# Kernel optimization log

Measured on AMD Instinct MI355X. Metric: run time of the kernel, lower is better.

## Reference

```python
import jax, jax.numpy as jnp
import numpy as np
from jax import lax

# pywt db8 decomposition low-pass filter (dec_lo), 16 taps
DB8_DEC_LO = jnp.array([
    -0.00011747678400228192, 0.0006754494059985568, -0.0003917403729959771,
    -0.00487035299301066, 0.008746094047015655, 0.013981027917015516,
    -0.04408825393106472, -0.01736930100202211, 0.128747426620186,
    0.00047248457399797254, -0.2840155429624281, -0.015829105256023893,
    0.5853546836548691, 0.6756307362980128, 0.3128715909144659,
    0.05441584224308161], dtype=jnp.float32)

FLEN = 16


def dwt2_ll(x):
    """LL band of pywt.dwt2(x, 'db8', mode='symmetric') for x [B,C,H,W].
    pywt dwt along an axis == symmetric pad by flen-1, full correlation with
    reversed dec_lo, take every other sample starting at offset 1."""
    B, C, H, W = x.shape
    f = DB8_DEC_LO[::-1]  # np.convolve flips the filter -> correlate with reversed
    xr = x.reshape(B * C, 1, H, W)
    # along W
    p = jnp.pad(xr, ((0, 0), (0, 0), (0, 0), (FLEN - 1, FLEN - 1)), mode='symmetric')[..., 1:]
    y = lax.conv_general_dilated(p, f.reshape(1, 1, 1, FLEN), (1, 2), 'VALID',
                                 dimension_numbers=('NCHW', 'OIHW', 'NCHW'))
    # along H
    p = jnp.pad(y, ((0, 0), (0, 0), (FLEN - 1, FLEN - 1), (0, 0)), mode='symmetric')[:, :, 1:, :]
    z = lax.conv_general_dilated(p, f.reshape(1, 1, FLEN, 1), (2, 1), 'VALID',
                                 dimension_numbers=('NCHW', 'OIHW', 'NCHW'))
    return z.reshape(B, C, z.shape[2], z.shape[3])


def setup_inputs() -> dict:
    key = jax.random.key(0)
    k1, k2, k3, k4 = jax.random.split(key, 4)
    B, C, H, W = 8, 128, 256, 256
    r = 16
    x = jax.random.normal(k1, (B, C, H, W), jnp.float32)
    conv_w = jax.random.normal(k2, (1, 2, 7, 7), jnp.float32) * 0.1  # SpatialAttention conv, no bias
    fc_w1 = jax.random.normal(k3, (C // r, C), jnp.float32) * (1.0 / np.sqrt(C))
    fc_w2 = jax.random.normal(k4, (C, C // r), jnp.float32) * (1.0 / np.sqrt(C // r))
    weight = jnp.array(0.0, dtype=jnp.float32)  # learnable fusion scalar
    return {"x": x, "conv_w": conv_w, "fc_w1": fc_w1, "fc_w2": fc_w2, "weight": weight}


def reference(x, conv_w, fc_w1, fc_w2, weight):
    # --- spatial attention ---
    avg = jnp.mean(x, axis=1, keepdims=True)
    mx = jnp.max(x, axis=1, keepdims=True)
    s = jnp.concatenate([avg, mx], axis=1)  # [B,2,H,W]
    attn = jax.nn.sigmoid(lax.conv_general_dilated(
        s, conv_w, (1, 1), ((3, 3), (3, 3)),
        dimension_numbers=('NCHW', 'OIHW', 'NCHW')))  # [B,1,H,W]
    spatial_out = x * attn
    # --- wavelet (frequency) attention; LL detached in the original ---
    ll = lax.stop_gradient(dwt2_ll(x))  # [B,C,H',W']
    y = jnp.mean(ll, axis=(2, 3))  # global avg pool -> [B,C]
    h = jax.nn.relu(y @ fc_w1.T)
    w = jax.nn.sigmoid(h @ fc_w2.T)[:, :, None, None]  # [B,C,1,1]
    wavelet_out = x * w
    # --- gated fusion ---
    alpha = jax.nn.sigmoid(weight)
    out = alpha * spatial_out + (1.0 - alpha) * wavelet_out
    return out, attn, w, alpha
```

## Files before the change

kernel.cpp:

```cpp
#include <hip/hip_runtime.h>
#include <math.h>

#define BB 8
#define CC 128
#define HH 256
#define WW 256
#define HWD 65536
#define NOUT (67108864)

#define ATTN_OFF ((size_t)NOUT)
#define W_OFF (ATTN_OFF + (size_t)BB * HWD)
#define ALPHA_OFF (W_OFF + (size_t)BB * CC)

__constant__ float g_declo[16] = {
    -0.00011747678400228192f, 0.0006754494059985568f, -0.0003917403729959771f,
    -0.00487035299301066f,    0.008746094047015655f,  0.013981027917015516f,
    -0.04408825393106472f,    -0.01736930100202211f,  0.128747426620186f,
    0.00047248457399797254f,  -0.2840155429624281f,   -0.015829105256023893f,
    0.5853546836548691f,      0.6756307362980128f,    0.3128715909144659f,
    0.05441584224308161f};

__device__ __forceinline__ float sigmoidf_(float v) {
    return 1.0f / (1.0f + expf(-v));
}

__device__ __forceinline__ float a_weight(int t) {
    float v = 0.0f;
    for (int k = (t & 1); k < 16; k += 2) v += g_declo[15 - k];
    if (t <= 13) {
        for (int k = 13 - t; k >= 0; k -= 2) v += g_declo[15 - k];
    }
    if (t >= 242) {
        for (int k = 257 - t; k < 16; k += 2) v += g_declo[15 - k];
    }
    return v;
}

__global__ __launch_bounds__(256) void pass1_kernel(
    const float* __restrict__ x, float* __restrict__ avg_s,
    float* __restrict__ max_s, float* __restrict__ partial) {
    const int blk = blockIdx.x;
    const int b = blk >> 8;
    const int h = blk & 255;
    const int tid = threadIdx.x;
    const int wv = tid >> 6;
    const int lane = tid & 63;

    __shared__ __align__(16) float a_sh[256];
    __shared__ float dotc[CC];
    __shared__ __align__(16) float lsum[4][256];
    __shared__ __align__(16) float lmax[4][256];
    __shared__ float T[4][64][17];

    a_sh[tid] = a_weight(tid);
    __syncthreads();

    const float4 a4 = reinterpret_cast<const float4*>(a_sh)[lane];
    const float ah = a_sh[h];

    float4 sum4 = {0.f, 0.f, 0.f, 0.f};
    float4 max4 = {-INFINITY, -INFINITY, -INFINITY, -INFINITY};

    const size_t base = (size_t)b * CC * HWD + (size_t)h * WW + (lane << 2);

    for (int g = 0; g < 2; ++g) {
        const int cbase = (wv << 5) + (g << 4);
        float dots[16];
#pragma unroll
        for (int i = 0; i < 16; ++i) {
            const float4 v = *reinterpret_cast<const float4*>(
                x + base + (size_t)(cbase + i) * HWD);
            dots[i] = a4.x * v.x + a4.y * v.y + a4.z * v.z + a4.w * v.w;
            sum4.x += v.x; sum4.y += v.y; sum4.z += v.z; sum4.w += v.w;
            max4.x = fmaxf(max4.x, v.x); max4.y = fmaxf(max4.y, v.y);
            max4.z = fmaxf(max4.z, v.z); max4.w = fmaxf(max4.w, v.w);
        }
#pragma unroll
        for (int i = 0; i < 16; ++i) T[wv][lane][i] = dots[i];
        const int cr = lane & 15;
        const int q = lane >> 4;
        float s = 0.f;
#pragma unroll
        for (int j = 0; j < 16; ++j) s += T[wv][(q << 4) + j][cr];
        s += __shfl_xor(s, 16, 64);
        s += __shfl_xor(s, 32, 64);
        if (lane < 16) dotc[cbase + lane] = s;
    }

    reinterpret_cast<float4*>(&lsum[wv][0])[lane] = sum4;
    reinterpret_cast<float4*>(&lmax[wv][0])[lane] = max4;
    __syncthreads();

    const int col = tid;
    const float s = lsum[0][col] + lsum[1][col] + lsum[2][col] + lsum[3][col];
    const float m = fmaxf(fmaxf(lmax[0][col], lmax[1][col]),
                          fmaxf(lmax[2][col], lmax[3][col]));
    const size_t po = (size_t)b * HWD + (size_t)h * WW + col;
    avg_s[po] = s * (1.0f / 128.0f);
    max_s[po] = m;
    if (tid < CC) partial[(size_t)blk * CC + tid] = dotc[tid] * ah;
}

__global__ __launch_bounds__(1024) void mlp_kernel(
    const float* __restrict__ partial, const float* __restrict__ fc_w1,
    const float* __restrict__ fc_w2, const float* __restrict__ weight,
    float* __restrict__ w_out, float* __restrict__ alpha_out) {
    const int b = blockIdx.x;
    const int t = threadIdx.x;
    const int c = t & 127;
    const int g = t >> 7;

    float acc = 0.0f;
    for (int h = g; h < HH; h += 8)
        acc += partial[((size_t)(b * HH + h)) * CC + c];

    __shared__ float red[8][CC];
    __shared__ float ysh[CC];
    __shared__ float hsh[8];
    red[g][c] = acc;
    __syncthreads();

    if (t < CC) {
        float y = 0.0f;
#pragma unroll
        for (int i = 0; i < 8; ++i) y += red[i][t];
        ysh[t] = y * (1.0f / (135.0f * 135.0f));
    }
    __syncthreads();
    if (t < 8) {
        float ha = 0.0f;
        for (int k = 0; k < CC; ++k) ha += ysh[k] * fc_w1[t * CC + k];
        hsh[t] = fmaxf(ha, 0.0f);
    }
    __syncthreads();
    if (t < CC) {
        float wa = 0.0f;
#pragma unroll
        for (int i = 0; i < 8; ++i) wa += hsh[i] * fc_w2[t * 8 + i];
        w_out[b * CC + t] = sigmoidf_(wa);
    }
    if (b == 0 && t == 0) alpha_out[0] = sigmoidf_(weight[0]);
}

__global__ __launch_bounds__(256) void conv_mix_kernel(
    const float* __restrict__ x, const float* __restrict__ avg_s,
    const float* __restrict__ max_s, const float* __restrict__ cw,
    const float* __restrict__ wvec, const float* __restrict__ alpha_p,
    float* __restrict__ attn_out, float* __restrict__ out) {
    const int blk = blockIdx.x;
    const int b = blk >> 8;
    const int h = blk & 255;
    const int tid = threadIdx.x;
    const int wv = tid >> 6;
    const int lane = tid & 63;

    __shared__ float k0[49], k1[49];
    __shared__ __align__(16) float sA[7][256];
    __shared__ __align__(16) float sM[7][256];
    __shared__ __align__(16) float att[256];
    __shared__ float wrow[CC];

    if (tid < 49) {
        k0[tid] = cw[tid];
        k1[tid] = cw[49 + tid];
    }
    if (tid < CC) wrow[tid] = wvec[b * CC + tid];

#pragma unroll
    for (int r = 0; r < 7; ++r) {
        const int ih = h - 3 + r;
        if (ih >= 0 && ih < HH) {
            sA[r][tid] = avg_s[(size_t)b * HWD + ih * WW + tid];
            sM[r][tid] = max_s[(size_t)b * HWD + ih * WW + tid];
        }
    }
    __syncthreads();

    float acc = 0.0f;
#pragma unroll
    for (int r = 0; r < 7; ++r) {
        const int ih = h - 3 + r;
        if (ih < 0 || ih >= HH) continue;
#pragma unroll
        for (int kw = 0; kw < 7; ++kw) {
            const int iw = tid + kw - 3;
            if (iw < 0 || iw >= WW) continue;
            acc = fmaf(k0[r * 7 + kw], sA[r][iw], acc);
            acc = fmaf(k1[r * 7 + kw], sM[r][iw], acc);
        }
    }
    const float av = sigmoidf_(acc);
    attn_out[(size_t)b * HWD + h * WW + tid] = av;
    att[tid] = av;
    __syncthreads();

    const float alpha = alpha_p[0];
    const float one_m = 1.0f - alpha;
    const float4 at4 = reinterpret_cast<const float4*>(att)[lane];
    const float4 aa4 = {alpha * at4.x, alpha * at4.y, alpha * at4.z,
                        alpha * at4.w};
    const size_t rowbase = (size_t)b * CC * HWD + (size_t)h * WW + (lane << 2);
#pragma unroll 4
    for (int ci = 0; ci < 32; ++ci) {
        const int c = (wv << 5) + ci;
        const float wc = one_m * wrow[c];
        const float4 x4 =
            *reinterpret_cast<const float4*>(x + rowbase + (size_t)c * HWD);
        float4 o;
        o.x = x4.x * (aa4.x + wc);
        o.y = x4.y * (aa4.y + wc);
        o.z = x4.z * (aa4.z + wc);
        o.w = x4.w * (aa4.w + wc);
        *reinterpret_cast<float4*>(out + rowbase + (size_t)c * HWD) = o;
    }
}

extern "C" void kernel_launch(void* const* d_in, const int* in_sizes, int n_in,
                              void* d_out, int out_size, void* d_ws,
                              size_t ws_size, hipStream_t stream) {
    const float* x = (const float*)d_in[0];
    const float* conv_w = (const float*)d_in[1];
    const float* fc_w1 = (const float*)d_in[2];
    const float* fc_w2 = (const float*)d_in[3];
    const float* weight = (const float*)d_in[4];

    float* out = (float*)d_out;
    float* attn_out = out + ATTN_OFF;
    float* w_out = out + W_OFF;
    float* alpha_out = out + ALPHA_OFF;

    float* wsf = (float*)d_ws;
    float* avg_s = wsf;
    float* max_s = avg_s + (size_t)BB * HWD;
    float* partial = max_s + (size_t)BB * HWD;

    pass1_kernel<<<BB * HH, 256, 0, stream>>>(x, avg_s, max_s, partial);
    mlp_kernel<<<BB, 1024, 0, stream>>>(partial, fc_w1, fc_w2, weight, w_out,
                                        alpha_out);
    conv_mix_kernel<<<BB * HH, 256, 0, stream>>>(x, avg_s, max_s, conv_w,
                                                 w_out, alpha_out, attn_out,
                                                 out);
}
```

Before: 543.0 us.

## Remap work so each wavefront owns one row across all channels

Both pass1 and conv_mix now launch 4 rows per block, with each wavefront handling one full row across all 128 channels rather than a quarter of the channels for one row. In pass1 this drops the cross-wave LDS reduction and the block sync, and the partial, avg and max results go straight out as float4 stores. In conv_mix the avg/max halo tiles (10 rows, zero-padded) are shared across 4 rows, and each thread computes 4 conv outputs. The mix loop walks channels in reverse, likely to reuse the tail of x still cached from pass1. The trade-off is 4x fewer blocks (512 per kernel) and longer serial per-wave loops, which may reduce latency hiding on a large GPU.

Result: no change. 541.3 us (-0.3%).

```diff
diff --git a/kernel.cpp b/kernel.cpp
--- a/kernel.cpp
+++ b/kernel.cpp
@@ -40,16 +40,14 @@
     const float* __restrict__ x, float* __restrict__ avg_s,
     float* __restrict__ max_s, float* __restrict__ partial) {
     const int blk = blockIdx.x;
-    const int b = blk >> 8;
-    const int h = blk & 255;
+    const int b = blk >> 6;
+    const int hq = blk & 63;
     const int tid = threadIdx.x;
-    const int wv = tid >> 6;
+    const int r = tid >> 6;
     const int lane = tid & 63;
+    const int h = (hq << 2) + r;
 
     __shared__ __align__(16) float a_sh[256];
-    __shared__ float dotc[CC];
-    __shared__ __align__(16) float lsum[4][256];
-    __shared__ __align__(16) float lmax[4][256];
     __shared__ float T[4][64][17];
 
     a_sh[tid] = a_weight(tid);
@@ -63,8 +61,8 @@
 
     const size_t base = (size_t)b * CC * HWD + (size_t)h * WW + (lane << 2);
 
-    for (int g = 0; g < 2; ++g) {
-        const int cbase = (wv << 5) + (g << 4);
+    for (int cg = 0; cg < 8; ++cg) {
+        const int cbase = cg << 4;
         float dots[16];
 #pragma unroll
         for (int i = 0; i < 16; ++i) {
@@ -76,29 +74,23 @@
             max4.z = fmaxf(max4.z, v.z); max4.w = fmaxf(max4.w, v.w);
         }
 #pragma unroll
-        for (int i = 0; i < 16; ++i) T[wv][lane][i] = dots[i];
+        for (int i = 0; i < 16; ++i) T[r][lane][i] = dots[i];
         const int cr = lane & 15;
         const int q = lane >> 4;
         float s = 0.f;
 #pragma unroll
-        for (int j = 0; j < 16; ++j) s += T[wv][(q << 4) + j][cr];
+        for (int j = 0; j < 16; ++j) s += T[r][(q << 4) + j][cr];
         s += __shfl_xor(s, 16, 64);
         s += __shfl_xor(s, 32, 64);
-        if (lane < 16) dotc[cbase + lane] = s;
-    }
-
-    reinterpret_cast<float4*>(&lsum[wv][0])[lane] = sum4;
-    reinterpret_cast<float4*>(&lmax[wv][0])[lane] = max4;
-    __syncthreads();
-
-    const int col = tid;
-    const float s = lsum[0][col] + lsum[1][col] + lsum[2][col] + lsum[3][col];
-    const float m = fmaxf(fmaxf(lmax[0][col], lmax[1][col]),
-                          fmaxf(lmax[2][col], lmax[3][col]));
-    const size_t po = (size_t)b * HWD + (size_t)h * WW + col;
-    avg_s[po] = s * (1.0f / 128.0f);
-    max_s[po] = m;
-    if (tid < CC) partial[(size_t)blk * CC + tid] = dotc[tid] * ah;
+        if (lane < 16)
+            partial[((size_t)(b * HH + h)) * CC + cbase + lane] = s * ah;
+    }
+
+    const size_t rowoff = (size_t)b * HWD + (size_t)h * WW;
+    float4 av = {sum4.x * (1.0f / 128.0f), sum4.y * (1.0f / 128.0f),
+                 sum4.z * (1.0f / 128.0f), sum4.w * (1.0f / 128.0f)};
+    reinterpret_cast<float4*>(avg_s + rowoff)[lane] = av;
+    reinterpret_cast<float4*>(max_s + rowoff)[lane] = max4;
 }
 
 __global__ __launch_bounds__(1024) void mlp_kernel(
@@ -148,70 +140,74 @@
     const float* __restrict__ wvec, const float* __restrict__ alpha_p,
     float* __restrict__ attn_out, float* __restrict__ out) {
     const int blk = blockIdx.x;
-    const int b = blk >> 8;
-    const int h = blk & 255;
+    const int b = blk >> 6;
+    const int hq = blk & 63;
     const int tid = threadIdx.x;
-    const int wv = tid >> 6;
+    const int r = tid >> 6;
     const int lane = tid & 63;
+    const int h = (hq << 2) + r;
+    const int c0 = lane << 2;
 
     __shared__ float k0[49], k1[49];
-    __shared__ __align__(16) float sA[7][256];
-    __shared__ __align__(16) float sM[7][256];
-    __shared__ __align__(16) float att[256];
+    __shared__ float sA[10][262];
+    __shared__ float sM[10][262];
     __shared__ float wrow[CC];
 
+    for (int i = tid; i < 2620; i += 256) {
+        (&sA[0][0])[i] = 0.f;
+        (&sM[0][0])[i] = 0.f;
+    }
     if (tid < 49) {
         k0[tid] = cw[tid];
         k1[tid] = cw[49 + tid];
     }
     if (tid < CC) wrow[tid] = wvec[b * CC + tid];
-
-#pragma unroll
-    for (int r = 0; r < 7; ++r) {
-        const int ih = h - 3 + r;
-        if (ih >= 0 && ih < HH) {
-            sA[r][tid] = avg_s[(size_t)b * HWD + ih * WW + tid];
-            sM[r][tid] = max_s[(size_t)b * HWD + ih * WW + tid];
+    __syncthreads();
+    for (int rr = 0; rr < 10; ++rr) {
+        const int row = (hq << 2) - 3 + rr;
+        if (row >= 0 && row < HH) {
+            sA[rr][3 + tid] = avg_s[(size_t)b * HWD + row * WW + tid];
+            sM[rr][3 + tid] = max_s[(size_t)b * HWD + row * WW + tid];
         }
     }
     __syncthreads();
 
-    float acc = 0.0f;
-#pragma unroll
-    for (int r = 0; r < 7; ++r) {
-        const int ih = h - 3 + r;
-        if (ih < 0 || ih >= HH) continue;
+    float acc0 = 0.f, acc1 = 0.f, acc2 = 0.f, acc3 = 0.f;
+#pragma unroll
+    for (int kh = 0; kh < 7; ++kh) {
 #pragma unroll
         for (int kw = 0; kw < 7; ++kw) {
-            const int iw = tid + kw - 3;
-            if (iw < 0 || iw >= WW) continue;
-            acc = fmaf(k0[r * 7 + kw], sA[r][iw], acc);
-            acc = fmaf(k1[r * 7 + kw], sM[r][iw], acc);
+            const float wa = k0[kh * 7 + kw];
+            const float wm = k1[kh * 7 + kw];
+            const float* pa = &sA[r + kh][c0 + kw];
+            const float* pm = &sM[r + kh][c0 + kw];
+            acc0 = fmaf(wa, pa[0], acc0); acc0 = fmaf(wm, pm[0], acc0);
+            acc1 = fmaf(wa, pa[1], acc1); acc1 = fmaf(wm, pm[1], acc1);
+            acc2 = fmaf(wa, pa[2], acc2); acc2 = fmaf(wm, pm[2], acc2);
+            acc3 = fmaf(wa, pa[3], acc3); acc3 = fmaf(wm, pm[3], acc3);
         }
     }
-    const float av = sigmoidf_(acc);
-    attn_out[(size_t)b * HWD + h * WW + tid] = av;
-    att[tid] = av;
-    __syncthreads();
+    const float4 att4 = {sigmoidf_(acc0), sigmoidf_(acc1), sigmoidf_(acc2),
+                         sigmoidf_(acc3)};
+    const size_t rowoff = (size_t)b * HWD + (size_t)h * WW + c0;
+    *reinterpret_cast<float4*>(attn_out + rowoff) = att4;
 
     const float alpha = alpha_p[0];
-    const float one_m = 1.0f - alpha;
-    const float4 at4 = reinterpret_cast<const float4*>(att)[lane];
-    const float4 aa4 = {alpha * at4.x, alpha * at4.y, alpha * at4.z,
-                        alpha * at4.w};
-    const size_t rowbase = (size_t)b * CC * HWD + (size_t)h * WW + (lane << 2);
-#pragma unroll 4
-    for (int ci = 0; ci < 32; ++ci) {
-        const int c = (wv << 5) + ci;
-        const float wc = one_m * wrow[c];
+    const float onem = 1.0f - alpha;
+    const float4 aa4 = {alpha * att4.x, alpha * att4.y, alpha * att4.z,
+                        alpha * att4.w};
+    const size_t base = (size_t)b * CC * HWD + (size_t)h * WW + c0;
+#pragma unroll 8
+    for (int ci = 127; ci >= 0; --ci) {
+        const float wc = onem * wrow[ci];
         const float4 x4 =
-            *reinterpret_cast<const float4*>(x + rowbase + (size_t)c * HWD);
+            *reinterpret_cast<const float4*>(x + base + (size_t)ci * HWD);
         float4 o;
         o.x = x4.x * (aa4.x + wc);
         o.y = x4.y * (aa4.y + wc);
         o.z = x4.z * (aa4.z + wc);
         o.w = x4.w * (aa4.w + wc);
-        *reinterpret_cast<float4*>(out + rowbase + (size_t)c * HWD) = o;
+        *reinterpret_cast<float4*>(out + base + (size_t)ci * HWD) = o;
     }
 }
 
@@ -234,10 +230,10 @@
     float* max_s = avg_s + (size_t)BB * HWD;
     float* partial = max_s + (size_t)BB * HWD;
 
-    pass1_kernel<<<BB * HH, 256, 0, stream>>>(x, avg_s, max_s, partial);
+    pass1_kernel<<<BB * 64, 256, 0, stream>>>(x, avg_s, max_s, partial);
     mlp_kernel<<<BB, 1024, 0, stream>>>(partial, fc_w1, fc_w2, weight, w_out,
                                         alpha_out);
-    conv_mix_kernel<<<BB * HH, 256, 0, stream>>>(x, avg_s, max_s, conv_w,
+    conv_mix_kernel<<<BB * 64, 256, 0, stream>>>(x, avg_s, max_s, conv_w,
                                                  w_out, alpha_out, attn_out,
                                                  out);
 }
```
